# Kernel optimization log

Measured on AMD Instinct MI355X. Metric: run time of the kernel, lower is better.

Reference implementation:

```python
import jax, jax.numpy as jnp
import numpy as np

Z_DIM = 2  # state dimension is hard-coded (fc1: Linear(2, H), fc3: Linear(H, 2))


def _mlp(z, W1, b1, W2, b2, W3, b3):
    # torch.nn.Linear: y = x @ W.T + b
    h = jax.nn.elu(z @ W1.T + b1)
    h = jax.nn.elu(h @ W2.T + b2)
    return h @ W3.T + b3


def setup_inputs() -> dict:
    key = jax.random.key(0)
    ks = jax.random.split(key, 8)
    B, H = 1_000_000, 64
    s_in = 1.0 / np.sqrt(Z_DIM)
    s_h = 1.0 / np.sqrt(H)
    u = lambda k, shp, s: jax.random.uniform(k, shp, jnp.float32, -s, s)
    return {
        "t": jax.random.normal(ks[0], (1,), jnp.float32),
        "z_and_logp": jax.random.normal(ks[1], (B, Z_DIM + 1), jnp.float32),
        "W1": u(ks[2], (H, Z_DIM), s_in),
        "b1": u(ks[3], (H,), s_in),
        "W2": u(ks[4], (H, H), s_h),
        "b2": u(ks[5], (H,), s_h),
        "W3": u(ks[6], (Z_DIM, H), s_h),
        "b3": u(ks[7], (Z_DIM,), s_h),
    }


def reference(t, z_and_logp, W1, b1, W2, b2, W3, b3):
    # t is an unused time argument (ODE solver interface).
    z = z_and_logp[:, :Z_DIM]  # [B, 2]; logp column is not used in forward
    f = lambda x: _mlp(x, W1, b1, W2, b2, W3, b3)

    # Exact Jacobian trace via forward-mode JVPs with unit tangents (Z_DIM=2,
    # so this small fixed loop mirrors the per-dim autograd loop in torch).
    dz_dt = None
    trace = jnp.zeros(z.shape[0], dtype=z.dtype)
    for i in range(Z_DIM):
        e = jnp.zeros_like(z).at[:, i].set(1.0)
        out, jz = jax.jvp(f, (z,), (e,))
        if dz_dt is None:
            dz_dt = out
        trace = trace + jz[:, i]

    dlogp_dt = -trace[:, None]  # [B, 1]
    return jnp.concatenate([dz_dt, dlogp_dt], axis=1)  # [B, 3]
```

## Files before the change

### kernel.cpp

```cpp
#include <hip/hip_runtime.h>
#include <hip/hip_bf16.h>


typedef short bf16x8 __attribute__((ext_vector_type(8)));
typedef float f32x4  __attribute__((ext_vector_type(4)));

static __device__ __forceinline__ short f2bf(float x) {
    __hip_bfloat16 b = __float2bfloat16(x);
    return __builtin_bit_cast(short, b);
}

__global__ __launch_bounds__(256) __attribute__((amdgpu_waves_per_eu(2, 2)))
void odefunc_mfma(const float* __restrict__ zin,
                  const float* __restrict__ W1, const float* __restrict__ b1,
                  const float* __restrict__ W2, const float* __restrict__ b2,
                  const float* __restrict__ W3, const float* __restrict__ b3,
                  float* __restrict__ out, int B, int ntiles)
{
    const int lane = threadIdx.x & 63;
    const int quad = lane >> 4;
    const int col  = lane & 15;

    const int wid    = blockIdx.x * (blockDim.x >> 6) + (threadIdx.x >> 6);
    const int nwaves = gridDim.x * (blockDim.x >> 6);

    bf16x8 aW2[4][2];
#pragma unroll
    for (int mt = 0; mt < 4; ++mt)
#pragma unroll
        for (int jt = 0; jt < 2; ++jt) {
            const float* p = W2 + (mt * 16 + col) * 64 + jt * 32 + quad * 8;
#pragma unroll
            for (int jj = 0; jj < 8; ++jj) aW2[mt][jt][jj] = f2bf(p[jj]);
        }

    float w0v[2][8], w1v[2][8], b1v[2][8];
#pragma unroll
    for (int jt = 0; jt < 2; ++jt)
#pragma unroll
        for (int jj = 0; jj < 8; ++jj) {
            int j = jt * 32 + quad * 8 + jj;
            w0v[jt][jj] = W1[2 * j];
            w1v[jt][jj] = W1[2 * j + 1];
            b1v[jt][jj] = b1[j];
        }

    float b2v[4][4], w30v[4][4], w31v[4][4];
#pragma unroll
    for (int mt = 0; mt < 4; ++mt)
#pragma unroll
        for (int i = 0; i < 4; ++i) {
            int k = mt * 16 + quad * 4 + i;
            b2v[mt][i]  = b2[k];
            w30v[mt][i] = W3[k];
            w31v[mt][i] = W3[64 + k];
        }
    const float b30 = b3[0], b31 = b3[1];
    const f32x4 zero4 = {0.f, 0.f, 0.f, 0.f};

    for (int t = wid; t < ntiles; t += nwaves) {
        int row = t * 16 + col;
        int rl = row < B ? row : B - 1;
        float z0 = zin[3 * rl + 0];
        float z1 = zin[3 * rl + 1];

        bf16x8 Ah[2], Au[2], Av[2];
#pragma unroll
        for (int jt = 0; jt < 2; ++jt)
#pragma unroll
            for (int jj = 0; jj < 8; ++jj) {
                float w0 = w0v[jt][jj], w1 = w1v[jt][jj];
                float a  = fmaf(w0, z0, fmaf(w1, z1, b1v[jt][jj]));
                float ex = __expf(fminf(a, 0.f));
                float h  = fmaxf(a, 0.f) + (ex - 1.f);
                Ah[jt][jj] = f2bf(h);
                Au[jt][jj] = f2bf(ex * w0);
                Av[jt][jj] = f2bf(ex * w1);
            }

        f32x4 accH[4], accU[4], accV[4];
#pragma unroll
        for (int mt = 0; mt < 4; ++mt) {
            accH[mt] = __builtin_amdgcn_mfma_f32_16x16x32_bf16(aW2[mt][0], Ah[0], zero4, 0, 0, 0);
            accH[mt] = __builtin_amdgcn_mfma_f32_16x16x32_bf16(aW2[mt][1], Ah[1], accH[mt], 0, 0, 0);
            accU[mt] = __builtin_amdgcn_mfma_f32_16x16x32_bf16(aW2[mt][0], Au[0], zero4, 0, 0, 0);
            accU[mt] = __builtin_amdgcn_mfma_f32_16x16x32_bf16(aW2[mt][1], Au[1], accU[mt], 0, 0, 0);
            accV[mt] = __builtin_amdgcn_mfma_f32_16x16x32_bf16(aW2[mt][0], Av[0], zero4, 0, 0, 0);
            accV[mt] = __builtin_amdgcn_mfma_f32_16x16x32_bf16(aW2[mt][1], Av[1], accV[mt], 0, 0, 0);
        }

        float o0 = 0.f, o1 = 0.f, trc = 0.f;
#pragma unroll
        for (int mt = 0; mt < 4; ++mt)
#pragma unroll
            for (int i = 0; i < 4; ++i) {
                float a2  = accH[mt][i] + b2v[mt][i];
                float ex2 = __expf(fminf(a2, 0.f));
                float hh  = fmaxf(a2, 0.f) + (ex2 - 1.f);
                o0  = fmaf(w30v[mt][i], hh, o0);
                o1  = fmaf(w31v[mt][i], hh, o1);
                trc = fmaf(ex2, fmaf(w30v[mt][i], accU[mt][i],
                                     w31v[mt][i] * accV[mt][i]), trc);
            }

        o0  += __shfl_xor(o0, 16);  o0  += __shfl_xor(o0, 32);
        o1  += __shfl_xor(o1, 16);  o1  += __shfl_xor(o1, 32);
        trc += __shfl_xor(trc, 16); trc += __shfl_xor(trc, 32);

        if (lane < 16 && row < B) {
            out[3 * row + 0] = o0 + b30;
            out[3 * row + 1] = o1 + b31;
            out[3 * row + 2] = -trc;
        }
    }
}

extern "C" void kernel_launch(void* const* d_in, const int* in_sizes, int n_in,
                              void* d_out, int out_size, void* d_ws, size_t ws_size,
                              hipStream_t stream) {
    const float* zin = (const float*)d_in[1];
    const float* W1  = (const float*)d_in[2];
    const float* b1  = (const float*)d_in[3];
    const float* W2  = (const float*)d_in[4];
    const float* b2  = (const float*)d_in[5];
    const float* W3  = (const float*)d_in[6];
    const float* b3  = (const float*)d_in[7];
    float* out = (float*)d_out;

    int B = in_sizes[1] / 3;
    int ntiles = (B + 15) / 16;
    int grid = 1024;
    odefunc_mfma<<<grid, 256, 0, stream>>>(zin, W1, b1, W2, b2, W3, b3,
                                           out, B, ntiles);
}
```

Before: 139.6 us.

## Process two row tiles per wave iteration to interleave MFMA chains

```diff
diff --git a/kernel.cpp b/kernel.cpp
--- a/kernel.cpp
+++ b/kernel.cpp
@@ -6,8 +6,9 @@
 typedef float f32x4  __attribute__((ext_vector_type(4)));
 
 static __device__ __forceinline__ short f2bf(float x) {
-    __hip_bfloat16 b = __float2bfloat16(x);
-    return __builtin_bit_cast(short, b);
+    unsigned u = __builtin_bit_cast(unsigned, x);
+    u = (u + 0x7FFFu + ((u >> 16) & 1u)) >> 16;
+    return (short)u;
 }
 
 __global__ __launch_bounds__(256) __attribute__((amdgpu_waves_per_eu(2, 2)))
@@ -45,72 +46,91 @@
             b1v[jt][jj] = b1[j];
         }
 
-    float b2v[4][4], w30v[4][4], w31v[4][4];
-#pragma unroll
-    for (int mt = 0; mt < 4; ++mt)
-#pragma unroll
-        for (int i = 0; i < 4; ++i) {
-            int k = mt * 16 + quad * 4 + i;
-            b2v[mt][i]  = b2[k];
-            w30v[mt][i] = W3[k];
-            w31v[mt][i] = W3[64 + k];
-        }
     const float b30 = b3[0], b31 = b3[1];
     const f32x4 zero4 = {0.f, 0.f, 0.f, 0.f};
 
-    for (int t = wid; t < ntiles; t += nwaves) {
-        int row = t * 16 + col;
-        int rl = row < B ? row : B - 1;
-        float z0 = zin[3 * rl + 0];
-        float z1 = zin[3 * rl + 1];
+    for (int t0 = wid * 2; t0 < ntiles; t0 += 2 * nwaves) {
+        const int t1 = t0 + 1;
+        int rowA = t0 * 16 + col;
+        int rowB = t1 * 16 + col;
+        int rA = rowA < B ? rowA : B - 1;
+        int rB = rowB < B ? rowB : B - 1;
+        float zA0 = zin[3 * rA + 0], zA1 = zin[3 * rA + 1];
+        float zB0 = zin[3 * rB + 0], zB1 = zin[3 * rB + 1];
 
-        bf16x8 Ah[2], Au[2], Av[2];
+        bf16x8 AhA[2], AuA[2], AvA[2], AhB[2], AuB[2], AvB[2];
 #pragma unroll
         for (int jt = 0; jt < 2; ++jt)
 #pragma unroll
             for (int jj = 0; jj < 8; ++jj) {
-                float w0 = w0v[jt][jj], w1 = w1v[jt][jj];
-                float a  = fmaf(w0, z0, fmaf(w1, z1, b1v[jt][jj]));
-                float ex = __expf(fminf(a, 0.f));
-                float h  = fmaxf(a, 0.f) + (ex - 1.f);
-                Ah[jt][jj] = f2bf(h);
-                Au[jt][jj] = f2bf(ex * w0);
-                Av[jt][jj] = f2bf(ex * w1);
+                float w0 = w0v[jt][jj], w1 = w1v[jt][jj], bb = b1v[jt][jj];
+                float aA  = fmaf(w0, zA0, fmaf(w1, zA1, bb));
+                float aB  = fmaf(w0, zB0, fmaf(w1, zB1, bb));
+                float exA = __expf(fminf(aA, 0.f));
+                float exB = __expf(fminf(aB, 0.f));
+                float hA  = fmaxf(aA, 0.f) + (exA - 1.f);
+                float hB  = fmaxf(aB, 0.f) + (exB - 1.f);
+                AhA[jt][jj] = f2bf(hA);   AhB[jt][jj] = f2bf(hB);
+                AuA[jt][jj] = f2bf(exA * w0); AuB[jt][jj] = f2bf(exB * w0);
+                AvA[jt][jj] = f2bf(exA * w1); AvB[jt][jj] = f2bf(exB * w1);
             }
 
-        f32x4 accH[4], accU[4], accV[4];
+        f32x4 aHA[4], aUA[4], aVA[4], aHB[4], aUB[4], aVB[4];
 #pragma unroll
         for (int mt = 0; mt < 4; ++mt) {
-            accH[mt] = __builtin_amdgcn_mfma_f32_16x16x32_bf16(aW2[mt][0], Ah[0], zero4, 0, 0, 0);
-            accH[mt] = __builtin_amdgcn_mfma_f32_16x16x32_bf16(aW2[mt][1], Ah[1], accH[mt], 0, 0, 0);
-            accU[mt] = __builtin_amdgcn_mfma_f32_16x16x32_bf16(aW2[mt][0], Au[0], zero4, 0, 0, 0);
-            accU[mt] = __builtin_amdgcn_mfma_f32_16x16x32_bf16(aW2[mt][1], Au[1], accU[mt], 0, 0, 0);
-            accV[mt] = __builtin_amdgcn_mfma_f32_16x16x32_bf16(aW2[mt][0], Av[0], zero4, 0, 0, 0);
-            accV[mt] = __builtin_amdgcn_mfma_f32_16x16x32_bf16(aW2[mt][1], Av[1], accV[mt], 0, 0, 0);
+            aHA[mt] = __builtin_amdgcn_mfma_f32_16x16x32_bf16(aW2[mt][0], AhA[0], zero4, 0, 0, 0);
+            aUA[mt] = __builtin_amdgcn_mfma_f32_16x16x32_bf16(aW2[mt][0], AuA[0], zero4, 0, 0, 0);
+            aVA[mt] = __builtin_amdgcn_mfma_f32_16x16x32_bf16(aW2[mt][0], AvA[0], zero4, 0, 0, 0);
+            aHB[mt] = __builtin_amdgcn_mfma_f32_16x16x32_bf16(aW2[mt][0], AhB[0], zero4, 0, 0, 0);
+            aUB[mt] = __builtin_amdgcn_mfma_f32_16x16x32_bf16(aW2[mt][0], AuB[0], zero4, 0, 0, 0);
+            aVB[mt] = __builtin_amdgcn_mfma_f32_16x16x32_bf16(aW2[mt][0], AvB[0], zero4, 0, 0, 0);
+            aHA[mt] = __builtin_amdgcn_mfma_f32_16x16x32_bf16(aW2[mt][1], AhA[1], aHA[mt], 0, 0, 0);
+            aUA[mt] = __builtin_amdgcn_mfma_f32_16x16x32_bf16(aW2[mt][1], AuA[1], aUA[mt], 0, 0, 0);
+            aVA[mt] = __builtin_amdgcn_mfma_f32_16x16x32_bf16(aW2[mt][1], AvA[1], aVA[mt], 0, 0, 0);
+            aHB[mt] = __builtin_amdgcn_mfma_f32_16x16x32_bf16(aW2[mt][1], AhB[1], aHB[mt], 0, 0, 0);
+            aUB[mt] = __builtin_amdgcn_mfma_f32_16x16x32_bf16(aW2[mt][1], AuB[1], aUB[mt], 0, 0, 0);
+            aVB[mt] = __builtin_amdgcn_mfma_f32_16x16x32_bf16(aW2[mt][1], AvB[1], aVB[mt], 0, 0, 0);
         }
 
-        float o0 = 0.f, o1 = 0.f, trc = 0.f;
+        float o0A = 0.f, o1A = 0.f, trA = 0.f;
+        float o0B = 0.f, o1B = 0.f, trB = 0.f;
 #pragma unroll
-        for (int mt = 0; mt < 4; ++mt)
+        for (int mt = 0; mt < 4; ++mt) {
+            int kb = mt * 16 + quad * 4;
+            f32x4 b2q  = *(const f32x4*)(b2 + kb);
+            f32x4 w30q = *(const f32x4*)(W3 + kb);
+            f32x4 w31q = *(const f32x4*)(W3 + 64 + kb);
 #pragma unroll
             for (int i = 0; i < 4; ++i) {
-                float a2  = accH[mt][i] + b2v[mt][i];
-                float ex2 = __expf(fminf(a2, 0.f));
-                float hh  = fmaxf(a2, 0.f) + (ex2 - 1.f);
-                o0  = fmaf(w30v[mt][i], hh, o0);
-                o1  = fmaf(w31v[mt][i], hh, o1);
-                trc = fmaf(ex2, fmaf(w30v[mt][i], accU[mt][i],
-                                     w31v[mt][i] * accV[mt][i]), trc);
+                float a2A  = aHA[mt][i] + b2q[i];
+                float a2B  = aHB[mt][i] + b2q[i];
+                float ex2A = __expf(fminf(a2A, 0.f));
+                float ex2B = __expf(fminf(a2B, 0.f));
+                float hhA  = fmaxf(a2A, 0.f) + (ex2A - 1.f);
+                float hhB  = fmaxf(a2B, 0.f) + (ex2B - 1.f);
+                o0A = fmaf(w30q[i], hhA, o0A);  o0B = fmaf(w30q[i], hhB, o0B);
+                o1A = fmaf(w31q[i], hhA, o1A);  o1B = fmaf(w31q[i], hhB, o1B);
+                trA = fmaf(ex2A, fmaf(w30q[i], aUA[mt][i], w31q[i] * aVA[mt][i]), trA);
+                trB = fmaf(ex2B, fmaf(w30q[i], aUB[mt][i], w31q[i] * aVB[mt][i]), trB);
             }
+        }
 
-        o0  += __shfl_xor(o0, 16);  o0  += __shfl_xor(o0, 32);
-        o1  += __shfl_xor(o1, 16);  o1  += __shfl_xor(o1, 32);
-        trc += __shfl_xor(trc, 16); trc += __shfl_xor(trc, 32);
+        o0A += __shfl_xor(o0A, 16); o0A += __shfl_xor(o0A, 32);
+        o1A += __shfl_xor(o1A, 16); o1A += __shfl_xor(o1A, 32);
+        trA += __shfl_xor(trA, 16); trA += __shfl_xor(trA, 32);
+        o0B += __shfl_xor(o0B, 16); o0B += __shfl_xor(o0B, 32);
+        o1B += __shfl_xor(o1B, 16); o1B += __shfl_xor(o1B, 32);
+        trB += __shfl_xor(trB, 16); trB += __shfl_xor(trB, 32);
 
-        if (lane < 16 && row < B) {
-            out[3 * row + 0] = o0 + b30;
-            out[3 * row + 1] = o1 + b31;
-            out[3 * row + 2] = -trc;
+        if (lane < 16 && rowA < B) {
+            out[3 * rowA + 0] = o0A + b30;
+            out[3 * rowA + 1] = o1A + b31;
+            out[3 * rowA + 2] = -trA;
+        }
+        if (lane < 16 && rowB < B) {
+            out[3 * rowB + 0] = o0B + b30;
+            out[3 * rowB + 1] = o1B + b31;
+            out[3 * rowB + 2] = -trB;
         }
     }
 }
```

Result: slower. 183.8 us (+31.7%).

## Reload layer weights per tile to cut registers and raise occupancy

Applied to the files above, without the earlier changes.

```diff
diff --git a/kernel.cpp b/kernel.cpp
--- a/kernel.cpp
+++ b/kernel.cpp
@@ -4,17 +4,36 @@
 
 typedef short bf16x8 __attribute__((ext_vector_type(8)));
 typedef float f32x4  __attribute__((ext_vector_type(4)));
+typedef int   i32x4  __attribute__((ext_vector_type(4)));
 
-static __device__ __forceinline__ short f2bf(float x) {
-    __hip_bfloat16 b = __float2bfloat16(x);
-    return __builtin_bit_cast(short, b);
+#if defined(__has_builtin)
+#if __has_builtin(__builtin_amdgcn_cvt_pk_bf16_f32)
+#define HAVE_PK_BF16 1
+#endif
+#endif
+
+#ifdef HAVE_PK_BF16
+typedef __bf16 bf16x2_t __attribute__((ext_vector_type(2)));
+static __device__ __forceinline__ int f2bf_pk(float a, float b) {
+    bf16x2_t r = __builtin_amdgcn_cvt_pk_bf16_f32(a, b);
+    return __builtin_bit_cast(int, r);
 }
+#else
+static __device__ __forceinline__ int f2bf_pk(float a, float b) {
+    unsigned ua = __builtin_bit_cast(unsigned, a);
+    unsigned ub = __builtin_bit_cast(unsigned, b);
+    ua = (ua + 0x7FFFu + ((ua >> 16) & 1u)) >> 16;
+    ub = (ub + 0x7FFFu + ((ub >> 16) & 1u)) & 0xFFFF0000u;
+    return (int)(ua | ub);
+}
+#endif
 
-__global__ __launch_bounds__(256) __attribute__((amdgpu_waves_per_eu(2, 2)))
+__global__ __launch_bounds__(256) __attribute__((amdgpu_waves_per_eu(3, 3)))
 void odefunc_mfma(const float* __restrict__ zin,
-                  const float* __restrict__ W1, const float* __restrict__ b1,
-                  const float* __restrict__ W2, const float* __restrict__ b2,
-                  const float* __restrict__ W3, const float* __restrict__ b3,
+                  const float* __restrict__ wpk,
+                  const float* __restrict__ W2,
+                  const float* __restrict__ b2, const float* __restrict__ W3,
+                  const float* __restrict__ b3,
                   float* __restrict__ out, int B, int ntiles)
 {
     const int lane = threadIdx.x & 63;
@@ -30,31 +49,13 @@
 #pragma unroll
         for (int jt = 0; jt < 2; ++jt) {
             const float* p = W2 + (mt * 16 + col) * 64 + jt * 32 + quad * 8;
+            i32x4 w;
 #pragma unroll
-            for (int jj = 0; jj < 8; ++jj) aW2[mt][jt][jj] = f2bf(p[jj]);
+            for (int p2 = 0; p2 < 4; ++p2)
+                w[p2] = f2bf_pk(p[2 * p2], p[2 * p2 + 1]);
+            aW2[mt][jt] = __builtin_bit_cast(bf16x8, w);
         }
 
-    float w0v[2][8], w1v[2][8], b1v[2][8];
-#pragma unroll
-    for (int jt = 0; jt < 2; ++jt)
-#pragma unroll
-        for (int jj = 0; jj < 8; ++jj) {
-            int j = jt * 32 + quad * 8 + jj;
-            w0v[jt][jj] = W1[2 * j];
-            w1v[jt][jj] = W1[2 * j + 1];
-            b1v[jt][jj] = b1[j];
-        }
-
-    float b2v[4][4], w30v[4][4], w31v[4][4];
-#pragma unroll
-    for (int mt = 0; mt < 4; ++mt)
-#pragma unroll
-        for (int i = 0; i < 4; ++i) {
-            int k = mt * 16 + quad * 4 + i;
-            b2v[mt][i]  = b2[k];
-            w30v[mt][i] = W3[k];
-            w31v[mt][i] = W3[64 + k];
-        }
     const float b30 = b3[0], b31 = b3[1];
     const f32x4 zero4 = {0.f, 0.f, 0.f, 0.f};
 
@@ -64,44 +65,64 @@
         float z0 = zin[3 * rl + 0];
         float z1 = zin[3 * rl + 1];
 
-        bf16x8 Ah[2], Au[2], Av[2];
-#pragma unroll
-        for (int jt = 0; jt < 2; ++jt)
-#pragma unroll
-            for (int jj = 0; jj < 8; ++jj) {
-                float w0 = w0v[jt][jj], w1 = w1v[jt][jj];
-                float a  = fmaf(w0, z0, fmaf(w1, z1, b1v[jt][jj]));
-                float ex = __expf(fminf(a, 0.f));
-                float h  = fmaxf(a, 0.f) + (ex - 1.f);
-                Ah[jt][jj] = f2bf(h);
-                Au[jt][jj] = f2bf(ex * w0);
-                Av[jt][jj] = f2bf(ex * w1);
-            }
+        const float* wp  = wpk;
+        const float* b2p = b2;
+        const float* w3p = W3;
+        asm volatile("" : "+s"(wp), "+s"(b2p), "+s"(w3p));
 
         f32x4 accH[4], accU[4], accV[4];
+
 #pragma unroll
-        for (int mt = 0; mt < 4; ++mt) {
-            accH[mt] = __builtin_amdgcn_mfma_f32_16x16x32_bf16(aW2[mt][0], Ah[0], zero4, 0, 0, 0);
-            accH[mt] = __builtin_amdgcn_mfma_f32_16x16x32_bf16(aW2[mt][1], Ah[1], accH[mt], 0, 0, 0);
-            accU[mt] = __builtin_amdgcn_mfma_f32_16x16x32_bf16(aW2[mt][0], Au[0], zero4, 0, 0, 0);
-            accU[mt] = __builtin_amdgcn_mfma_f32_16x16x32_bf16(aW2[mt][1], Au[1], accU[mt], 0, 0, 0);
-            accV[mt] = __builtin_amdgcn_mfma_f32_16x16x32_bf16(aW2[mt][0], Av[0], zero4, 0, 0, 0);
-            accV[mt] = __builtin_amdgcn_mfma_f32_16x16x32_bf16(aW2[mt][1], Av[1], accV[mt], 0, 0, 0);
+        for (int jt = 0; jt < 2; ++jt) {
+            i32x4 Ah, Au, Av;
+#pragma unroll
+            for (int p2 = 0; p2 < 4; ++p2) {
+                int j0 = jt * 32 + quad * 8 + 2 * p2;
+                f32x4 c0 = *(const f32x4*)(wp + 4 * j0);
+                f32x4 c1 = *(const f32x4*)(wp + 4 * j0 + 4);
+                float a0 = fmaf(c0.x, z0, fmaf(c0.y, z1, c0.z));
+                float a1 = fmaf(c1.x, z0, fmaf(c1.y, z1, c1.z));
+                float e0 = __expf(fminf(a0, 0.f));
+                float e1 = __expf(fminf(a1, 0.f));
+                float h0 = fmaxf(a0, 0.f) + (e0 - 1.f);
+                float h1 = fmaxf(a1, 0.f) + (e1 - 1.f);
+                Ah[p2] = f2bf_pk(h0, h1);
+                Au[p2] = f2bf_pk(e0 * c0.x, e1 * c1.x);
+                Av[p2] = f2bf_pk(e0 * c0.y, e1 * c1.y);
+            }
+            bf16x8 bh = __builtin_bit_cast(bf16x8, Ah);
+            bf16x8 bu = __builtin_bit_cast(bf16x8, Au);
+            bf16x8 bv = __builtin_bit_cast(bf16x8, Av);
+
+#pragma unroll
+            for (int mt = 0; mt < 4; ++mt) {
+                accH[mt] = __builtin_amdgcn_mfma_f32_16x16x32_bf16(
+                    aW2[mt][jt], bh, jt == 0 ? zero4 : accH[mt], 0, 0, 0);
+                accU[mt] = __builtin_amdgcn_mfma_f32_16x16x32_bf16(
+                    aW2[mt][jt], bu, jt == 0 ? zero4 : accU[mt], 0, 0, 0);
+                accV[mt] = __builtin_amdgcn_mfma_f32_16x16x32_bf16(
+                    aW2[mt][jt], bv, jt == 0 ? zero4 : accV[mt], 0, 0, 0);
+            }
         }
 
         float o0 = 0.f, o1 = 0.f, trc = 0.f;
 #pragma unroll
-        for (int mt = 0; mt < 4; ++mt)
+        for (int mt = 0; mt < 4; ++mt) {
+            int kb = mt * 16 + quad * 4;
+            f32x4 b2q  = *(const f32x4*)(b2p + kb);
+            f32x4 w30q = *(const f32x4*)(w3p + kb);
+            f32x4 w31q = *(const f32x4*)(w3p + 64 + kb);
 #pragma unroll
             for (int i = 0; i < 4; ++i) {
-                float a2  = accH[mt][i] + b2v[mt][i];
+                float a2  = accH[mt][i] + b2q[i];
                 float ex2 = __expf(fminf(a2, 0.f));
                 float hh  = fmaxf(a2, 0.f) + (ex2 - 1.f);
-                o0  = fmaf(w30v[mt][i], hh, o0);
-                o1  = fmaf(w31v[mt][i], hh, o1);
-                trc = fmaf(ex2, fmaf(w30v[mt][i], accU[mt][i],
-                                     w31v[mt][i] * accV[mt][i]), trc);
+                o0  = fmaf(w30q[i], hh, o0);
+                o1  = fmaf(w31q[i], hh, o1);
+                trc = fmaf(ex2, fmaf(w30q[i], accU[mt][i],
+                                     w31q[i] * accV[mt][i]), trc);
             }
+        }
 
         o0  += __shfl_xor(o0, 16);  o0  += __shfl_xor(o0, 32);
         o1  += __shfl_xor(o1, 16);  o1  += __shfl_xor(o1, 32);
@@ -112,6 +133,19 @@
             out[3 * row + 1] = o1 + b31;
             out[3 * row + 2] = -trc;
         }
+    }
+}
+
+__global__ void pack_w1(const float* __restrict__ W1,
+                        const float* __restrict__ b1,
+                        float* __restrict__ ws)
+{
+    int j = threadIdx.x;
+    if (j < 64) {
+        ws[4 * j + 0] = W1[2 * j + 0];
+        ws[4 * j + 1] = W1[2 * j + 1];
+        ws[4 * j + 2] = b1[j];
+        ws[4 * j + 3] = 0.f;
     }
 }
 
@@ -126,10 +160,12 @@
     const float* W3  = (const float*)d_in[6];
     const float* b3  = (const float*)d_in[7];
     float* out = (float*)d_out;
+    float* wsf = (float*)d_ws;
 
     int B = in_sizes[1] / 3;
     int ntiles = (B + 15) / 16;
-    int grid = 1024;
-    odefunc_mfma<<<grid, 256, 0, stream>>>(zin, W1, b1, W2, b2, W3, b3,
-                                           out, B, ntiles);
+
+    pack_w1<<<1, 64, 0, stream>>>(W1, b1, wsf);
+    odefunc_mfma<<<768, 256, 0, stream>>>(zin, wsf, W2, b2, W3, b3,
+                                          out, B, ntiles);
 }
```

Measured after the change: 163.2 us. 16.9% more time.
